# Kernel tuning notes

Measured on AMD Instinct MI355X. Metric: run time of the kernel, lower is better.

The kernel has to match this reference:

```python
import jax, jax.numpy as jnp
import numpy as np

B, L, DM, H = 2, 2048, 1024, 16
D = DM // H  # head_dim = key_dim = 64


def setup_inputs() -> dict:
    key = jax.random.key(0)
    ks = jax.random.split(key, 6)
    w = 0.02
    return {
        "x": jax.random.normal(ks[0], (B, L, DM), dtype=jnp.float32),
        "wq_attn": jax.random.normal(ks[1], (DM, H * D), dtype=jnp.float32) * w,
        "wk_attn": jax.random.normal(ks[2], (DM, H * D), dtype=jnp.float32) * w,
        "wq_rel": jax.random.normal(ks[3], (DM, H * D), dtype=jnp.float32) * w,
        "wk_rel": jax.random.normal(ks[4], (DM, H * D), dtype=jnp.float32) * w,
        "wo": jax.random.normal(ks[5], (H * D, H * D), dtype=jnp.float32) * w,
    }


def reference(x, wq_attn, wk_attn, wq_rel, wk_rel, wo):
    b, l, dm = x.shape
    # projections -> (B, L, H, D); MHA so n_kv_heads == n_heads, no repeat_kv
    q = (x @ wq_attn).reshape(b, l, H, D)
    k = (x @ wk_attn).reshape(b, l, H, D)
    qr = (x @ wq_rel).reshape(b, l, H, D)
    kr = (x @ wk_rel).reshape(b, l, H, D)

    scale = D ** -0.5  # SDPA default: 1/sqrt(query key_dim)
    scores = jnp.einsum("blhd,bmhd->bhlm", q, k) * scale  # (B, H, L, L)
    causal = jnp.tril(jnp.ones((l, l), dtype=bool))
    scores = jnp.where(causal, scores, -jnp.inf)
    attn = jax.nn.softmax(scores, axis=-1)

    # attend over relational keys, then Hadamard with relational queries
    attended_kr = jnp.einsum("bhlm,bmhd->blhd", attn, kr)  # (B, L, H, D)
    attended_relations = qr * attended_kr                    # (B, L, H, D)

    out = attended_relations.reshape(b, l, H * D) @ wo       # (B, L, d_model)
    return out
```

## Files before the change

### kernel.cpp

```cpp
#include <hip/hip_runtime.h>
#include <stdint.h>


typedef __attribute__((ext_vector_type(4))) float floatx4;
typedef __attribute__((ext_vector_type(8))) short shortx8;
typedef __attribute__((ext_vector_type(4))) short shortx4;

__device__ __forceinline__ unsigned short f2bf(float f) {
    unsigned u = __float_as_uint(f);
    u += 0x7fffu + ((u >> 16) & 1u);
    return (unsigned short)(u >> 16);
}
__device__ __forceinline__ float bf2f(unsigned short s) {
    return __uint_as_float(((unsigned)s) << 16);
}
__device__ __forceinline__ float exp2fast(float x) {
#if __has_builtin(__builtin_amdgcn_exp2f)
    return __builtin_amdgcn_exp2f(x);
#else
    return __expf(x * 0.69314718056f);
#endif
}
__device__ __forceinline__ unsigned pkbf(float e0, float e1) {
    return __builtin_amdgcn_perm(__float_as_uint(e1), __float_as_uint(e0), 0x07060302u);
}
__device__ __forceinline__ floatx4 mfma16(shortx4 a, shortx4 b, floatx4 c) {
#if __has_builtin(__builtin_amdgcn_mfma_f32_16x16x16bf16_1k)
    return __builtin_amdgcn_mfma_f32_16x16x16bf16_1k(a, b, c, 0, 0, 0);
#else
    shortx8 a8 = {a[0], a[1], a[2], a[3], 0, 0, 0, 0};
    shortx8 b8 = {b[0], b[1], b[2], b[3], 0, 0, 0, 0};
    return __builtin_amdgcn_mfma_f32_16x16x32_bf16(a8, b8, c, 0, 0, 0);
#endif
}
__device__ __forceinline__ void gll16(const void* g, void* l) {
    __builtin_amdgcn_global_load_lds(
        (const __attribute__((address_space(1))) unsigned int*)g,
        (__attribute__((address_space(3))) unsigned int*)l, 16, 0, 0);
}

__global__ void k_cvt_x(const float* __restrict__ x, unsigned short* __restrict__ xb) {
    int i = (blockIdx.x * 256 + threadIdx.x) * 4;
    float4 v = *(const float4*)(x + i);
    ushort4 o;
    o.x = f2bf(v.x); o.y = f2bf(v.y); o.z = f2bf(v.z); o.w = f2bf(v.w);
    *(ushort4*)(xb + i) = o;
}

__global__ __launch_bounds__(256) void k_cvt_w5(const float* __restrict__ wq,
                                                const float* __restrict__ wk,
                                                const float* __restrict__ wqr,
                                                const float* __restrict__ wkr,
                                                const float* __restrict__ wo,
                                                unsigned short* __restrict__ wcatT,
                                                unsigned short* __restrict__ wotT) {
    __shared__ unsigned short Tl[64 * 65];
    const int t = threadIdx.x;
    const int kt = blockIdx.x * 64, nt = blockIdx.y * 64;
    const int z = blockIdx.z;
    const float* W = (z == 0) ? wq : (z == 1) ? wk : (z == 2) ? wqr : (z == 3) ? wkr : wo;
    unsigned short* outT = (z < 4) ? (wcatT + (size_t)z * 1024 * 1024) : wotT;
    const float scale = (z == 0) ? 0.18033688f : 1.0f;
    {
        const int kl = t >> 3, nc = (t & 7) * 8;
        const float* src = W + (size_t)(kt + kl) * 1024 + nt + nc;
        float a[8], b[8];
        *(float4*)(a)     = *(const float4*)(src);
        *(float4*)(a + 4) = *(const float4*)(src + 4);
        *(float4*)(b)     = *(const float4*)(src + 32 * 1024);
        *(float4*)(b + 4) = *(const float4*)(src + 32 * 1024 + 4);
#pragma unroll
        for (int i = 0; i < 8; ++i) {
            Tl[kl * 65 + nc + i]        = f2bf(a[i] * scale);
            Tl[(kl + 32) * 65 + nc + i] = f2bf(b[i] * scale);
        }
    }
    __syncthreads();
    {
        const int n = t >> 2, kc = (t & 3) * 16;
        shortx8 o0, o1;
#pragma unroll
        for (int i = 0; i < 8; ++i) {
            o0[i] = (short)Tl[(kc + i) * 65 + n];
            o1[i] = (short)Tl[(kc + 8 + i) * 65 + n];
        }
        unsigned short* dst = outT + (size_t)(nt + n) * 1024 + kt + kc;
        *(shortx8*)(dst)     = o0;
        *(shortx8*)(dst + 8) = o1;
    }
}

__global__ __launch_bounds__(256) void k_trans(const unsigned short* __restrict__ qcat,
                                               unsigned short* __restrict__ krT) {
    __shared__ unsigned short Tl[64 * 65];
    const int t = threadIdx.x;
    const int mt = blockIdx.x * 64;
    const int bh = blockIdx.y;
    const int b = bh >> 4, h = bh & 15;
    {
        const int ml = t >> 3, dc = (t & 7) * 8;
        const unsigned short* src =
            qcat + ((size_t)b * 2048 + mt + ml) * 4096 + 3072 + h * 64 + dc;
        shortx8 v0 = *(const shortx8*)(src);
        shortx8 v1 = *(const shortx8*)(src + (size_t)32 * 4096);
#pragma unroll
        for (int i = 0; i < 8; ++i) {
            Tl[ml * 65 + dc + i]        = (unsigned short)v0[i];
            Tl[(ml + 32) * 65 + dc + i] = (unsigned short)v1[i];
        }
    }
    __syncthreads();
    {
        const int d = t >> 2, mc = (t & 3) * 16;
        shortx8 o0, o1;
#pragma unroll
        for (int i = 0; i < 8; ++i) {
            o0[i] = (short)Tl[(mc + i) * 65 + d];
            o1[i] = (short)Tl[(mc + 8 + i) * 65 + d];
        }
        unsigned short* dst = krT + ((size_t)bh * 64 + d) * 2048 + mt + mc;
        *(shortx8*)(dst)     = o0;
        *(shortx8*)(dst + 8) = o1;
    }
}

__global__ __launch_bounds__(256) void k_gemm_bt(const unsigned short* __restrict__ A,
                                                 const unsigned short* __restrict__ Bt,
                                                 unsigned short* __restrict__ C,
                                                 int N, int K) {
    __shared__ alignas(16) unsigned short As[2][128 * 32];
    __shared__ alignas(16) unsigned short Bs[2][128 * 32];
    const int t = threadIdx.x;
    const int lane = t & 63, wv = t >> 6;
    const int ln = lane & 15, quad = lane >> 4;
    const int wm = wv >> 1, wn = wv & 1;
    const int bm = blockIdx.y * 128, bn = blockIdx.x * 128;

    floatx4 acc[4][4] = {};

    const int srow = t >> 2;
    const int sc = (t & 3) ^ ((srow >> 1) & 3);
    const unsigned short* ga0 = A + (size_t)(bm + srow) * K + sc * 8;
    const unsigned short* ga1 = ga0 + (size_t)64 * K;
    const unsigned short* gb0 = Bt + (size_t)(bn + srow) * K + sc * 8;
    const unsigned short* gb1 = gb0 + (size_t)64 * K;

    gll16(ga0, &As[0][wv * 512]);
    gll16(ga1, &As[0][2048 + wv * 512]);
    gll16(gb0, &Bs[0][wv * 512]);
    gll16(gb1, &Bs[0][2048 + wv * 512]);

    const int sw = (ln >> 1) & 3;
    int cur = 0;
    for (int k0 = 0; k0 < K; k0 += 32, cur ^= 1) {
        __syncthreads();
        const int nk = k0 + 32;
        if (nk < K) {
            gll16(ga0 + nk, &As[cur ^ 1][wv * 512]);
            gll16(ga1 + nk, &As[cur ^ 1][2048 + wv * 512]);
            gll16(gb0 + nk, &Bs[cur ^ 1][wv * 512]);
            gll16(gb1 + nk, &Bs[cur ^ 1][2048 + wv * 512]);
        }
        shortx8 af[4], bfr[4];
#pragma unroll
        for (int i = 0; i < 4; ++i)
            af[i] = *(const shortx8*)(&As[cur][(wm * 64 + i * 16 + ln) * 32 + ((quad ^ sw) * 8)]);
#pragma unroll
        for (int j = 0; j < 4; ++j)
            bfr[j] = *(const shortx8*)(&Bs[cur][(wn * 64 + j * 16 + ln) * 32 + ((quad ^ sw) * 8)]);
#pragma unroll
        for (int i = 0; i < 4; ++i)
#pragma unroll
            for (int j = 0; j < 4; ++j)
                acc[i][j] = __builtin_amdgcn_mfma_f32_16x16x32_bf16(af[i], bfr[j], acc[i][j], 0, 0, 0);
    }

#pragma unroll
    for (int i = 0; i < 4; ++i)
#pragma unroll
        for (int j = 0; j < 4; ++j)
#pragma unroll
            for (int r = 0; r < 4; ++r) {
                int row = bm + wm * 64 + i * 16 + quad * 4 + r;
                int col = bn + wn * 64 + j * 16 + ln;
                C[(size_t)row * N + col] = f2bf(acc[i][j][r]);
            }
}

__global__ __launch_bounds__(256) void k_gemm_n64(const unsigned short* __restrict__ A,
                                                  const unsigned short* __restrict__ Bt,
                                                  float* __restrict__ C,
                                                  int N, int K) {
    __shared__ alignas(16) unsigned short As[2][128 * 32];
    __shared__ alignas(16) unsigned short Bs[2][64 * 32];
    const int t = threadIdx.x;
    const int lane = t & 63, wv = t >> 6;
    const int ln = lane & 15, quad = lane >> 4;
    const int bm = blockIdx.y * 128, bn = blockIdx.x * 64;

    floatx4 acc[2][4] = {};

    const int srow = t >> 2;
    const int sc = (t & 3) ^ ((srow >> 1) & 3);
    const unsigned short* ga0 = A + (size_t)(bm + srow) * K + sc * 8;
    const unsigned short* ga1 = ga0 + (size_t)64 * K;
    const unsigned short* gb0 = Bt + (size_t)(bn + srow) * K + sc * 8;

    gll16(ga0, &As[0][wv * 512]);
    gll16(ga1, &As[0][2048 + wv * 512]);
    gll16(gb0, &Bs[0][wv * 512]);

    const int sw = (ln >> 1) & 3;
    int cur = 0;
    for (int k0 = 0; k0 < K; k0 += 32, cur ^= 1) {
        __syncthreads();
        const int nk = k0 + 32;
        if (nk < K) {
            gll16(ga0 + nk, &As[cur ^ 1][wv * 512]);
            gll16(ga1 + nk, &As[cur ^ 1][2048 + wv * 512]);
            gll16(gb0 + nk, &Bs[cur ^ 1][wv * 512]);
        }
        shortx8 af[2], bfr[4];
#pragma unroll
        for (int i = 0; i < 2; ++i)
            af[i] = *(const shortx8*)(&As[cur][(wv * 32 + i * 16 + ln) * 32 + ((quad ^ sw) * 8)]);
#pragma unroll
        for (int j = 0; j < 4; ++j)
            bfr[j] = *(const shortx8*)(&Bs[cur][(j * 16 + ln) * 32 + ((quad ^ sw) * 8)]);
#pragma unroll
        for (int i = 0; i < 2; ++i)
#pragma unroll
            for (int j = 0; j < 4; ++j)
                acc[i][j] = __builtin_amdgcn_mfma_f32_16x16x32_bf16(af[i], bfr[j], acc[i][j], 0, 0, 0);
    }

#pragma unroll
    for (int i = 0; i < 2; ++i)
#pragma unroll
        for (int j = 0; j < 4; ++j)
#pragma unroll
            for (int r = 0; r < 4; ++r) {
                int row = bm + wv * 32 + i * 16 + quad * 4 + r;
                int col = bn + j * 16 + ln;
                C[(size_t)row * N + col] = acc[i][j][r];
            }
}

__global__ __launch_bounds__(256, 4) void k_attn(const unsigned short* __restrict__ qcat,
                                                 const unsigned short* __restrict__ krT,
                                                 unsigned short* __restrict__ ar) {
    __shared__ alignas(16) unsigned short Kl[2][64 * 64];
    __shared__ alignas(16) unsigned short Rl[2][64 * 64];

    const int t = threadIdx.x;
    const int lane = t & 63, w = t >> 6;
    const int ln = lane & 15, quad = lane >> 4;
    const int bh = blockIdx.y;
    const int b = bh >> 4, h = bh & 15;
    const int qx = blockIdx.x;
    const int qt = (qx & 1) ? 31 - (qx >> 1) : (qx >> 1);
    const int l0 = qt * 64;
    const size_t baserow = (size_t)b * 2048;

    const int qrow = l0 + w * 16 + ln;
    const unsigned short* qp = qcat + (baserow + qrow) * 4096 + h * 64 + quad * 8;
    const shortx8 aq0 = *(const shortx8*)(qp);
    const shortx8 aq1 = *(const shortx8*)(qp + 32);

    floatx4 acc_o[4] = {};
    float lsum = 0.f;

    const int srow = t >> 3;
    const int sc = (t & 7) ^ (srow & 7);
    const unsigned short* gK = qcat + (baserow + srow) * 4096 + 1024 + h * 64 + sc * 8;
    const unsigned short* gR = krT + ((size_t)bh * 64 + srow) * 2048 + sc * 8;

    auto stage = [&](int kt, int buf) {
        gll16(gK + (size_t)(kt * 64) * 4096,      &Kl[buf][w * 512]);
        gll16(gK + (size_t)(kt * 64 + 32) * 4096, &Kl[buf][2048 + w * 512]);
        gll16(gR + kt * 64,                       &Rl[buf][w * 512]);
        gll16(gR + (size_t)32 * 2048 + kt * 64,   &Rl[buf][2048 + w * 512]);
    };

    stage(0, 0);
    const int swz = ln & 7;
    int cur = 0;
    for (int kt = 0; kt <= qt; ++kt, cur ^= 1) {
        __syncthreads();
        if (kt < qt) stage(kt + 1, cur ^ 1);
        const unsigned short* Kc = Kl[cur];
        const unsigned short* Rc = Rl[cur];
        const bool diag = (kt == qt);

        shortx4 pk[4];
#pragma unroll
        for (int jk = 0; jk < 4; ++jk) {
            const int kr0 = (jk * 16 + ln) * 64;
            shortx8 kf0 = *(const shortx8*)(Kc + kr0 + ((quad ^ swz) * 8));
            shortx8 kf1 = *(const shortx8*)(Kc + kr0 + (((4 + quad) ^ swz) * 8));
            floatx4 z = {0.f, 0.f, 0.f, 0.f};
            z = __builtin_amdgcn_mfma_f32_16x16x32_bf16(kf0, aq0, z, 0, 0, 0);
            z = __builtin_amdgcn_mfma_f32_16x16x32_bf16(kf1, aq1, z, 0, 0, 0);
            float e0 = exp2fast(z[0]);
            float e1 = exp2fast(z[1]);
            float e2 = exp2fast(z[2]);
            float e3 = exp2fast(z[3]);
            if (diag) {
                const int keyb = kt * 64 + jk * 16 + quad * 4;
                e0 = (keyb + 0 > qrow) ? 0.f : e0;
                e1 = (keyb + 1 > qrow) ? 0.f : e1;
                e2 = (keyb + 2 > qrow) ? 0.f : e2;
                e3 = (keyb + 3 > qrow) ? 0.f : e3;
            }
            lsum += (e0 + e1) + (e2 + e3);
            struct U2 { unsigned a, b; } u{pkbf(e0, e1), pkbf(e2, e3)};
            pk[jk] = __builtin_bit_cast(shortx4, u);
        }

#pragma unroll
        for (int jk = 0; jk < 4; ++jk) {
            const int cm = jk * 2 + (quad >> 1);
#pragma unroll
            for (int jd = 0; jd < 4; ++jd) {
                shortx4 krf = *(const shortx4*)(Rc + (jd * 16 + ln) * 64 +
                                                ((cm ^ swz) * 8) + (quad & 1) * 4);
                acc_o[jd] = mfma16(krf, pk[jk], acc_o[jd]);
            }
        }
    }

    float s = lsum;
    s += __shfl_xor(s, 16);
    s += __shfl_xor(s, 32);
    const float inv = 1.0f / s;
    const unsigned short* qr = qcat + (baserow + qrow) * 4096 + 2048 + h * 64;
    unsigned short* arow = ar + (baserow + qrow) * 1024 + h * 64;
#pragma unroll
    for (int jd = 0; jd < 4; ++jd) {
        const int d0 = jd * 16 + quad * 4;
        shortx4 qv = *(const shortx4*)(qr + d0);
        shortx4 o;
#pragma unroll
        for (int r = 0; r < 4; ++r)
            o[r] = (short)f2bf(acc_o[jd][r] * inv * bf2f((unsigned short)qv[r]));
        *(shortx4*)(arow + d0) = o;
    }
}

extern "C" void kernel_launch(void* const* d_in, const int* in_sizes, int n_in,
                              void* d_out, int out_size, void* d_ws, size_t ws_size,
                              hipStream_t stream) {
    const float* x   = (const float*)d_in[0];
    const float* wq  = (const float*)d_in[1];
    const float* wk  = (const float*)d_in[2];
    const float* wqr = (const float*)d_in[3];
    const float* wkr = (const float*)d_in[4];
    const float* wo  = (const float*)d_in[5];
    float* out = (float*)d_out;

    unsigned short* xb    = (unsigned short*)d_ws;
    unsigned short* wcatT = xb + (size_t)4096 * 1024;
    unsigned short* qcat  = wcatT + (size_t)4096 * 1024;
    unsigned short* wotT  = qcat + (size_t)4096 * 4096;
    unsigned short* krT   = wcatT;
    unsigned short* arb   = xb;

    k_cvt_x<<<4096, 256, 0, stream>>>(x, xb);
    k_cvt_w5<<<dim3(16, 16, 5), 256, 0, stream>>>(wq, wk, wqr, wkr, wo, wcatT, wotT);
    k_gemm_bt<<<dim3(32, 32), 256, 0, stream>>>(xb, wcatT, qcat, 4096, 1024);
    k_trans<<<dim3(32, 32), 256, 0, stream>>>(qcat, krT);
    k_attn<<<dim3(32, 32), 256, 0, stream>>>(qcat, krT, arb);
    k_gemm_n64<<<dim3(16, 32), 256, 0, stream>>>(arb, wotT, out, 1024, 1024);
}
```

Before: 215.7 us.

## Split attention work across waves by key chunk with LDS reduction

The attention kernel now gives each wave one 16-key slice of every 64-key tile and has it cover all 64 query rows, where before each wave owned 16 query rows and looped over all keys. Each wave loads K and relational-K fragments from LDS once per tile instead of per query chunk, which cuts LDS read traffic. The partial outputs and row sums are then combined across the four waves through shared memory. The price is 64 accumulator registers per thread (occupancy hint lowered from 4 to 2) and an extra multi-barrier reduction epilogue. The grid is also flattened and remapped so neighbouring blocks interleave heads.

```diff
diff --git a/kernel.cpp b/kernel.cpp
--- a/kernel.cpp
+++ b/kernel.cpp
@@ -246,29 +246,35 @@
             }
 }
 
-__global__ __launch_bounds__(256, 4) void k_attn(const unsigned short* __restrict__ qcat,
+__global__ __launch_bounds__(256, 2) void k_attn(const unsigned short* __restrict__ qcat,
                                                  const unsigned short* __restrict__ krT,
                                                  unsigned short* __restrict__ ar) {
     __shared__ alignas(16) unsigned short Kl[2][64 * 64];
     __shared__ alignas(16) unsigned short Rl[2][64 * 64];
+    __shared__ float Ls[4][4][16];
 
     const int t = threadIdx.x;
     const int lane = t & 63, w = t >> 6;
     const int ln = lane & 15, quad = lane >> 4;
-    const int bh = blockIdx.y;
+    const int flat = blockIdx.x;
+    const int bh = (flat & 7) * 4 + ((flat >> 3) & 3);
+    const int qts = flat >> 5;
+    const int qt = (qts & 1) ? 31 - (qts >> 1) : (qts >> 1);
     const int b = bh >> 4, h = bh & 15;
-    const int qx = blockIdx.x;
-    const int qt = (qx & 1) ? 31 - (qx >> 1) : (qx >> 1);
     const int l0 = qt * 64;
     const size_t baserow = (size_t)b * 2048;
 
-    const int qrow = l0 + w * 16 + ln;
-    const unsigned short* qp = qcat + (baserow + qrow) * 4096 + h * 64 + quad * 8;
-    const shortx8 aq0 = *(const shortx8*)(qp);
-    const shortx8 aq1 = *(const shortx8*)(qp + 32);
-
-    floatx4 acc_o[4] = {};
-    float lsum = 0.f;
+    shortx8 aq[4][2];
+#pragma unroll
+    for (int qc = 0; qc < 4; ++qc) {
+        const unsigned short* qp =
+            qcat + (baserow + l0 + qc * 16 + ln) * 4096 + h * 64 + quad * 8;
+        aq[qc][0] = *(const shortx8*)(qp);
+        aq[qc][1] = *(const shortx8*)(qp + 32);
+    }
+
+    floatx4 acc_o[4][4] = {};
+    float lsum[4] = {0.f, 0.f, 0.f, 0.f};
 
     const int srow = t >> 3;
     const int sc = (t & 7) ^ (srow & 7);
@@ -284,6 +290,8 @@
 
     stage(0, 0);
     const int swz = ln & 7;
+    const int krow = (w * 16 + ln) * 64;
+    const int cmw = w * 2 + (quad >> 1);
     int cur = 0;
     for (int kt = 0; kt <= qt; ++kt, cur ^= 1) {
         __syncthreads();
@@ -292,58 +300,108 @@
         const unsigned short* Rc = Rl[cur];
         const bool diag = (kt == qt);
 
+        shortx8 kf0 = *(const shortx8*)(Kc + krow + ((quad ^ swz) * 8));
+        shortx8 kf1 = *(const shortx8*)(Kc + krow + (((4 + quad) ^ swz) * 8));
+        shortx4 krf[4];
+#pragma unroll
+        for (int jd = 0; jd < 4; ++jd)
+            krf[jd] = *(const shortx4*)(Rc + (jd * 16 + ln) * 64 +
+                                        ((cmw ^ swz) * 8) + (quad & 1) * 4);
+
+        const int keyb = kt * 64 + w * 16 + quad * 4;
         shortx4 pk[4];
 #pragma unroll
-        for (int jk = 0; jk < 4; ++jk) {
-            const int kr0 = (jk * 16 + ln) * 64;
-            shortx8 kf0 = *(const shortx8*)(Kc + kr0 + ((quad ^ swz) * 8));
-            shortx8 kf1 = *(const shortx8*)(Kc + kr0 + (((4 + quad) ^ swz) * 8));
+        for (int qc = 0; qc < 4; ++qc) {
             floatx4 z = {0.f, 0.f, 0.f, 0.f};
-            z = __builtin_amdgcn_mfma_f32_16x16x32_bf16(kf0, aq0, z, 0, 0, 0);
-            z = __builtin_amdgcn_mfma_f32_16x16x32_bf16(kf1, aq1, z, 0, 0, 0);
+            z = __builtin_amdgcn_mfma_f32_16x16x32_bf16(kf0, aq[qc][0], z, 0, 0, 0);
+            z = __builtin_amdgcn_mfma_f32_16x16x32_bf16(kf1, aq[qc][1], z, 0, 0, 0);
             float e0 = exp2fast(z[0]);
             float e1 = exp2fast(z[1]);
             float e2 = exp2fast(z[2]);
             float e3 = exp2fast(z[3]);
             if (diag) {
-                const int keyb = kt * 64 + jk * 16 + quad * 4;
-                e0 = (keyb + 0 > qrow) ? 0.f : e0;
-                e1 = (keyb + 1 > qrow) ? 0.f : e1;
-                e2 = (keyb + 2 > qrow) ? 0.f : e2;
-                e3 = (keyb + 3 > qrow) ? 0.f : e3;
+                const int q = l0 + qc * 16 + ln;
+                e0 = (keyb + 0 > q) ? 0.f : e0;
+                e1 = (keyb + 1 > q) ? 0.f : e1;
+                e2 = (keyb + 2 > q) ? 0.f : e2;
+                e3 = (keyb + 3 > q) ? 0.f : e3;
             }
-            lsum += (e0 + e1) + (e2 + e3);
+            lsum[qc] += (e0 + e1) + (e2 + e3);
             struct U2 { unsigned a, b; } u{pkbf(e0, e1), pkbf(e2, e3)};
-            pk[jk] = __builtin_bit_cast(shortx4, u);
-        }
-
-#pragma unroll
-        for (int jk = 0; jk < 4; ++jk) {
-            const int cm = jk * 2 + (quad >> 1);
+            pk[qc] = __builtin_bit_cast(shortx4, u);
+        }
+
+#pragma unroll
+        for (int qc = 0; qc < 4; ++qc)
+#pragma unroll
+            for (int jd = 0; jd < 4; ++jd)
+                acc_o[qc][jd] = mfma16(krf[jd], pk[qc], acc_o[qc][jd]);
+    }
+
+#pragma unroll
+    for (int qc = 0; qc < 4; ++qc) {
+        float s = lsum[qc];
+        s += __shfl_xor(s, 16);
+        s += __shfl_xor(s, 32);
+        lsum[qc] = s;
+    }
+    if (lane < 16) {
+#pragma unroll
+        for (int qc = 0; qc < 4; ++qc) Ls[w][qc][lane] = lsum[qc];
+    }
+
+    __syncthreads();
+    float* redA = (float*)&Kl[0][0];
+    float* redB = (float*)&Rl[0][0];
+    if (w >= 2) {
+        float* dst = (w == 2) ? redA : redB;
+#pragma unroll
+        for (int qc = 0; qc < 4; ++qc)
+#pragma unroll
+            for (int jd = 0; jd < 4; ++jd)
+                *(floatx4*)(dst + ((qc * 4 + jd) * 64 + lane) * 4) = acc_o[qc][jd];
+    }
+    __syncthreads();
+    if (w < 2) {
+        const float* src = (w == 0) ? redA : redB;
+#pragma unroll
+        for (int qc = 0; qc < 4; ++qc)
+#pragma unroll
+            for (int jd = 0; jd < 4; ++jd)
+                acc_o[qc][jd] += *(const floatx4*)(src + ((qc * 4 + jd) * 64 + lane) * 4);
+    }
+    __syncthreads();
+    if (w == 1) {
+#pragma unroll
+        for (int qc = 0; qc < 4; ++qc)
+#pragma unroll
+            for (int jd = 0; jd < 4; ++jd)
+                *(floatx4*)(redA + ((qc * 4 + jd) * 64 + lane) * 4) = acc_o[qc][jd];
+    }
+    __syncthreads();
+    if (w == 0) {
+        float inv[4];
+#pragma unroll
+        for (int qc = 0; qc < 4; ++qc)
+            inv[qc] = 1.0f / (Ls[0][qc][ln] + Ls[1][qc][ln] + Ls[2][qc][ln] + Ls[3][qc][ln]);
+#pragma unroll
+        for (int qc = 0; qc < 4; ++qc) {
+            const int q = l0 + qc * 16 + ln;
+            const unsigned short* qr = qcat + (baserow + q) * 4096 + 2048 + h * 64;
+            unsigned short* arow = ar + (baserow + q) * 1024 + h * 64;
 #pragma unroll
             for (int jd = 0; jd < 4; ++jd) {
-                shortx4 krf = *(const shortx4*)(Rc + (jd * 16 + ln) * 64 +
-                                                ((cm ^ swz) * 8) + (quad & 1) * 4);
-                acc_o[jd] = mfma16(krf, pk[jk], acc_o[jd]);
+                floatx4 a = acc_o[qc][jd];
+                a += *(const floatx4*)(redA + ((qc * 4 + jd) * 64 + lane) * 4);
+                const int d0 = jd * 16 + quad * 4;
+                shortx4 qv = *(const shortx4*)(qr + d0);
+                shortx4 o;
+#pragma unroll
+                for (int r = 0; r < 4; ++r)
+                    o[r] = (short)f2bf(a[r] * inv[qc] * bf2f((unsigned short)qv[r]));
+                *(shortx4*)(arow + d0) = o;
             }
         }
-    }
-
-    float s = lsum;
-    s += __shfl_xor(s, 16);
-    s += __shfl_xor(s, 32);
-    const float inv = 1.0f / s;
-    const unsigned short* qr = qcat + (baserow + qrow) * 4096 + 2048 + h * 64;
-    unsigned short* arow = ar + (baserow + qrow) * 1024 + h * 64;
-#pragma unroll
-    for (int jd = 0; jd < 4; ++jd) {
-        const int d0 = jd * 16 + quad * 4;
-        shortx4 qv = *(const shortx4*)(qr + d0);
-        shortx4 o;
-#pragma unroll
-        for (int r = 0; r < 4; ++r)
-            o[r] = (short)f2bf(acc_o[jd][r] * inv * bf2f((unsigned short)qv[r]));
-        *(shortx4*)(arow + d0) = o;
     }
 }
 
@@ -369,6 +427,6 @@
     k_cvt_w5<<<dim3(16, 16, 5), 256, 0, stream>>>(wq, wk, wqr, wkr, wo, wcatT, wotT);
     k_gemm_bt<<<dim3(32, 32), 256, 0, stream>>>(xb, wcatT, qcat, 4096, 1024);
     k_trans<<<dim3(32, 32), 256, 0, stream>>>(qcat, krT);
-    k_attn<<<dim3(32, 32), 256, 0, stream>>>(qcat, krT, arb);
+    k_attn<<<1024, 256, 0, stream>>>(qcat, krT, arb);
     k_gemm_n64<<<dim3(16, 32), 256, 0, stream>>>(arb, wotT, out, 1024, 1024);
 }
```

New measurement: 201.7 us. 6.5% less time.
